# Kernel tuning notes

Hardware: AMD Instinct MI355X
Metric: run time of the kernel (lower is better)

The kernel has to match this reference:

```python
import jax, jax.numpy as jnp
import numpy as np

LS, BS, N_HID, N_PART, T, D_IN, M = 2, 16, 256, 512, 16, 64, 1
MID = N_PART // 2


def setup_inputs() -> dict:
    key = jax.random.key(0)
    ks = jax.random.split(key, 12)
    s = 0.1
    inp = {}
    inp["x"] = jax.random.normal(ks[0], (BS, T, D_IN), jnp.float32)
    inp["y"] = jax.random.normal(ks[1], (BS,), jnp.float32)
    inp["particles"] = jax.random.normal(ks[2], (LS, BS, N_HID, N_PART), jnp.float32)
    inp["weights"] = jnp.full((BS, N_PART), 1.0 / N_PART, jnp.float32)
    inp["q"] = jnp.asarray(1.0, jnp.float32)
    inp["e"] = jnp.asarray(0.1, jnp.float32)
    inp["r"] = jnp.asarray(0.5, jnp.float32)
    inp["Wih0"] = jax.random.normal(ks[3], (4 * N_HID, D_IN), jnp.float32) * s
    inp["Whh0"] = jax.random.normal(ks[4], (4 * N_HID, N_HID), jnp.float32) * s
    inp["b0"] = jnp.zeros((4 * N_HID,), jnp.float32)
    inp["Wih1"] = jax.random.normal(ks[5], (4 * N_HID, N_HID), jnp.float32) * s
    inp["Whh1"] = jax.random.normal(ks[6], (4 * N_HID, N_HID), jnp.float32) * s
    inp["b1"] = jnp.zeros((4 * N_HID,), jnp.float32)
    inp["Wh"] = jax.random.normal(ks[7], (M, N_HID), jnp.float32) * s
    inp["bh"] = jnp.zeros((M,), jnp.float32)
    inp["eps_h"] = jax.random.normal(ks[8], (MID, LS, BS, N_HID), jnp.float32)
    inp["eps_c"] = jax.random.normal(ks[9], (MID, LS, BS, N_HID), jnp.float32)
    u = jax.random.uniform(ks[10], (BS, 2, MID), jnp.float32, minval=1e-6, maxval=1.0)
    inp["gumbel"] = -jnp.log(-jnp.log(u))  # Gumbel noise for multinomial resampling
    return inp


def _lstm(x, h0, c0, Wih0, Whh0, b0, Wih1, Whh1, b1, q2, e2, eps_h, eps_c):
    # x: [bs,T,d]; h0,c0: [ls,bs,n]. Two-layer LSTM, noise added to final states.
    xs = jnp.swapaxes(x, 0, 1)  # [T,bs,d]

    def make_step(Wih, Whh, b):
        def step(carry, xt):
            h, c = carry
            g = xt @ Wih.T + h @ Whh.T + b
            i, f, gg, o = jnp.split(g, 4, axis=-1)
            c2 = jax.nn.sigmoid(f) * c + jax.nn.sigmoid(i) * jnp.tanh(gg)
            h2 = jax.nn.sigmoid(o) * jnp.tanh(c2)
            return (h2, c2), h2
        return step

    (hA, cA), out0 = jax.lax.scan(make_step(Wih0, Whh0, b0), (h0[0], c0[0]), xs)
    (hB, cB), out1 = jax.lax.scan(make_step(Wih1, Whh1, b1), (h0[1], c0[1]), out0)
    hT = jnp.stack([hA, hB]) + jnp.sqrt(q2) * eps_h
    cT = jnp.stack([cA, cB]) + jnp.sqrt(e2) * eps_c
    return jnp.swapaxes(out1, 0, 1), hT, cT


def _obs(u_last, Wh, bh):  # u_last: [bs,n,N] -> [bs,m,N]
    return jnp.einsum('mn,bnN->bmN', Wh, u_last) + bh[None, :, None]


def _estimate(Y, w, r):
    # Y: [bs,m,N], w: [bs,N]
    w_sum = jnp.sum(w, -1)
    W_mu = jnp.einsum('bmN,bN->bm', Y, w) / w_sum[:, None]
    cen = Y - W_mu[:, :, None]
    cov = jnp.einsum('bmN,bkN->bmk', cen, cen) / (Y.shape[-1] - 1)
    cov = cov + jnp.eye(Y.shape[1], dtype=Y.dtype) * (r * r)
    return W_mu, cov


def _inv_logdet(sig):
    m = sig.shape[-1]
    sig = sig + 1e-6 * jnp.eye(m, dtype=sig.dtype)
    L = jnp.linalg.cholesky(sig)
    inv_sig = jnp.linalg.inv(jnp.swapaxes(L, -2, -1)) @ jnp.linalg.inv(L)
    logdet = jnp.linalg.slogdet(sig)[1]
    return inv_sig, logdet


def reference(x, y, particles, weights, q, e, r, Wih0, Whh0, b0, Wih1, Whh1, b1, Wh, bh, eps_h, eps_c, gumbel):
    q2, e2 = q * q, e * e  # noise is squared before the transition (TransitionF)
    # ---- forecast_PF: particle i is h, particle i+MID is c ----
    h_parts = jnp.moveaxis(particles[..., :MID], -1, 0)  # [MID,ls,bs,n]
    c_parts = jnp.moveaxis(particles[..., MID:], -1, 0)
    step_fn = jax.vmap(lambda h0, c0, eh, ec: _lstm(x, h0, c0, Wih0, Whh0, b0, Wih1, Whh1, b1, q2, e2, eh, ec)[1:])
    hN, cN = step_fn(h_parts, c_parts, eps_h, eps_c)
    pr = jnp.moveaxis(jnp.concatenate([hN, cN], 0), 0, -1)  # [ls,bs,n,N]

    # ---- torch_PF weight update ----
    w = jnp.log(weights)
    Y = _obs(pr[-1], Wh, bh)  # [bs,m,N]
    W_mu_e, sig_e = _estimate(Y, w, r)  # NOTE: original passes LOG weights here (faithful)
    inv_sig, logdet = _inv_logdet(sig_e)
    w_sum = jnp.sum(w, -1)
    Wmu2 = Y * w[:, None, :] / w_sum[:, None, None]  # elementwise, as in w_likelihood
    innov = y[:, None, None] - Wmu2  # [bs,m,N]
    quad = jnp.einsum('bmN,bmk,bkN->bN', innov, inv_sig, innov)
    new_w = w + (-0.5 * logdet[:, None] - 0.5 * quad)
    # original: new_w -= log(sum(exp(new_w))) where python-sum reduces dim 0 -> [N]
    new_w = new_w - jnp.log(jnp.sum(jnp.exp(new_w), axis=0))[None, :]
    new_w = jnp.exp(new_w)

    # ---- per-batch, per-half soft resampling when neff < N/4 ----
    def resample_half(p, wh, g):  # p [ls,n,MID], wh [MID], g [MID]
        neff = 1.0 / jnp.sum(wh * wh)
        do = neff < (N_PART / 4.0)
        soft = 0.5 * wh + 0.5 / MID
        idx = jnp.argsort(-(jnp.log(soft) + g))  # weighted sample w/o replacement (Gumbel top-k)
        p_r = p[:, :, idx]
        lw = jnp.log(wh / soft)
        w_r = jnp.exp(lw - jax.nn.logsumexp(lw))
        return jnp.where(do, p_r, p), jnp.where(do, w_r, wh)

    def per_batch(p_b, w_b, g_b):  # p_b [ls,n,N], w_b [N], g_b [2,MID]
        p1, w1 = resample_half(p_b[:, :, :MID], w_b[:MID], g_b[0])
        p2, w2 = resample_half(p_b[:, :, MID:], w_b[MID:], g_b[1])
        return jnp.concatenate([p1, p2], -1), jnp.concatenate([w1, w2], 0)

    pf, wf = jax.vmap(per_batch, in_axes=(1, 0, 0), out_axes=(1, 0))(pr, new_w, gumbel)

    # ---- train=True branch: estimate / likelihood / NIS on filtered ensemble ----
    Yf = _obs(pf[-1], Wh, bh)
    W_mu, sig = _estimate(Yf, wf, r)
    inv_s, ld = _inv_logdet(sig)
    inn = y[:, None] - W_mu  # [bs,m]
    qf = jnp.einsum('bm,bmk,bk->b', inn, inv_s, inn)
    l = jnp.sum(-0.5 * ld - 0.5 * qf)
    nis = jnp.mean(qf)
    return W_mu, sig, pf, wf, l, nis
```

## Files before the change

### kernel.cpp

```cpp
#include <hip/hip_runtime.h>
#include <hip/hip_bf16.h>
#include <math.h>

#define LSN 2
#define BSN 16
#define NH 256
#define NP 512
#define MIDP 256
#define TTN 16
#define DIN 64
#define NCH 4096
#define GW 1024
#define PRS 268
#define BUFSZ 36864

typedef _Float16 f16;
typedef _Float16 f16x8 __attribute__((ext_vector_type(8)));
typedef float f32x4 __attribute__((ext_vector_type(4)));

__device__ __forceinline__ float fsig(float x){ return 1.0f/(1.0f+expf(-x)); }

__device__ __forceinline__ float brsum512(float v, float* red){
  int tid = threadIdx.x;
  red[tid]=v; __syncthreads();
  for (int s=256; s>0; s>>=1){ if (tid<s) red[tid]+=red[tid+s]; __syncthreads(); }
  float r = red[0]; __syncthreads(); return r;
}
__device__ __forceinline__ float brsum(float v, float* red){
  int tid = threadIdx.x;
  red[tid]=v; __syncthreads();
  for (int s=128; s>0; s>>=1){ if (tid<s) red[tid]+=red[tid+s]; __syncthreads(); }
  float r = red[0]; __syncthreads(); return r;
}

__device__ __forceinline__ int gsrow(int jp){
  return ((jp>>5)&3)*NH + (jp>>7)*32 + (jp&31);
}

__global__ __launch_bounds__(256) void k_prep_all(
    const float* __restrict__ Whh0, const float* __restrict__ Wih1,
    const float* __restrict__ Whh1, const float* __restrict__ b1,
    const float* __restrict__ x, const float* __restrict__ Wih0,
    const float* __restrict__ b0, const float* __restrict__ part,
    f16* __restrict__ W0i, f16* __restrict__ W1c, float* __restrict__ b1i,
    float* __restrict__ xW0,
    f16* __restrict__ h0, f16* __restrict__ h1,
    float* __restrict__ c0, float* __restrict__ c1)
{
  __shared__ float lh[64][65];
  __shared__ float lcv[64][65];
  int bid = blockIdx.x;
  int tid = threadIdx.x;
  if (bid < 1024){
    int jp = bid; int srow = gsrow(jp); int t = tid;
    W0i[(size_t)jp*NH + t]        = (f16)Whh0[(size_t)srow*NH + t];
    W1c[(size_t)jp*512 + t]       = (f16)Wih1[(size_t)srow*NH + t];
    W1c[(size_t)jp*512 + 256 + t] = (f16)Whh1[(size_t)srow*NH + t];
    if (t==0) b1i[jp] = b1[srow];
  } else if (bid < 1280){
    int row = bid - 1024;
    float* xr = lh[0];
    if (tid < DIN) xr[tid] = x[(size_t)row*DIN + tid];
    __syncthreads();
    int n = tid;
    for (int q=0;q<4;++q){
      int wrow = q*NH + n;
      float acc = b0[wrow];
      #pragma unroll 8
      for (int d=0; d<DIN; ++d) acc += xr[d] * Wih0[(size_t)wrow*DIN + d];
      int jhat = (n>>5)*128 + q*32 + (n&31);
      xW0[(size_t)row*GW + jhat] = acc;
    }
  } else {
    int idx = bid - 1280;
    int xb = idx & 15, b = (idx>>4)&15, l = idx>>8;
    int i0 = (xb >> 2)*64, n0 = (xb & 3)*64;
    #pragma unroll
    for (int rep=0; rep<16; ++rep){
      int nn = rep*4 + (tid>>6);
      int ii = tid & 63;
      size_t rowb = ((size_t)(l*BSN + b)*NH + n0 + nn)*NP;
      lh[nn][ii]  = part[rowb + i0 + ii];
      lcv[nn][ii] = part[rowb + MIDP + i0 + ii];
    }
    __syncthreads();
    f16* h = l ? h1 : h0;
    float* c = l ? c1 : c0;
    #pragma unroll
    for (int rep=0; rep<16; ++rep){
      int ii = rep*4 + (tid>>6);
      int nn = tid & 63;
      size_t chain = (size_t)b*256 + i0 + ii;
      h[chain*NH + n0 + nn] = (f16)lh[nn][ii];
      c[chain*NH + n0 + nn] = lcv[nn][ii];
    }
  }
}

struct StepCfg {
  const f16* A1; const f16* A2;
  float* C; f16* Hout;
  int layer; int t; int is_last;
};

__global__ __launch_bounds__(256) void k_step2(
    StepCfg cfgA, StepCfg cfgB,
    const f16* __restrict__ W0i, const f16* __restrict__ W1c,
    const float* __restrict__ xw0, const float* __restrict__ b1i,
    float* __restrict__ pr, const float* __restrict__ eps_h, const float* __restrict__ eps_c,
    const float* __restrict__ qp, const float* __restrict__ ep)
{
  __shared__ __align__(16) char smem[2*BUFSZ];

  const int bid = blockIdx.x;
  const int xcd = bid & 7, jj = bid >> 3;
  const int mloc = jj & 3, y = (jj >> 2) & 7, z = (jj >> 5) & 1;
  const int mt = xcd*4 + mloc;
  const int m0 = mt * 128;

  const StepCfg cfg = z ? cfgB : cfgA;
  const int layer  = cfg.layer;
  const int Kt     = layer ? 512 : 256;
  const int nslice = layer ? 8 : 4;
  const f16* W     = layer ? W1c : W0i;

  const int tid = threadIdx.x;
  const int lane = tid & 63, wid = tid >> 6;
  const int lr = lane >> 4, lc = lane & 15;
  const int wm = wid * 32;
  const int bb = mt >> 1;

  float cold[2][2][4];
  #pragma unroll
  for (int mi=0; mi<2; ++mi)
    #pragma unroll
    for (int mh=0; mh<2; ++mh)
      #pragma unroll
      for (int r=0; r<4; ++r)
        cold[mi][mh][r] = cfg.C[(size_t)(m0 + wm + mi*16 + lr*4 + r)*NH + y*32 + mh*16 + lc];

  f32x4 acc[2][8];
  #pragma unroll
  for (int mi=0;mi<2;++mi)
    #pragma unroll
    for (int ni=0;ni<8;++ni) acc[mi][ni] = (f32x4){0.f,0.f,0.f,0.f};

  const int srow = tid >> 1, sseg = (tid & 1)*32;

  float4 ra0,ra1,ra2,ra3, rb0,rb1,rb2,rb3;
  auto loadslice = [&](int ks){
    const f16* Ab; int ka;
    if (layer==1 && ks>=4){ Ab = cfg.A2; ka = (ks-4)*64; } else { Ab = cfg.A1; ka = ks*64; }
    const float4* sa = (const float4*)(Ab + (size_t)(m0+srow)*NH + ka + sseg);
    const float4* sb = (const float4*)(W + (size_t)(y*128+srow)*Kt + (size_t)ks*64 + sseg);
    ra0=sa[0]; ra1=sa[1]; ra2=sa[2]; ra3=sa[3];
    rb0=sb[0]; rb1=sb[1]; rb2=sb[2]; rb3=sb[3];
  };
  auto writeslice = [&](int buf){
    f16* base = (f16*)(smem + buf*BUFSZ);
    float4* da = (float4*)(base + srow*72 + sseg);
    da[0]=ra0; da[1]=ra1; da[2]=ra2; da[3]=ra3;
    float4* db = (float4*)(base + 128*72 + srow*72 + sseg);
    db[0]=rb0; db[1]=rb1; db[2]=rb2; db[3]=rb3;
  };

  loadslice(0);
  writeslice(0);
  __syncthreads();
  for (int ks=0; ks<nslice; ++ks){
    const int cur = ks & 1;
    const bool more = (ks+1) < nslice;
    if (more) loadslice(ks+1);
    const f16* bufA = (const f16*)(smem + cur*BUFSZ);
    const f16* bufB = bufA + 128*72;
    #pragma unroll
    for (int k2=0;k2<2;++k2){
      const int koff = k2*32 + lr*8;
      f16x8 a0 = *(const f16x8*)(bufA + (wm +  0 + lc)*72 + koff);
      f16x8 a1 = *(const f16x8*)(bufA + (wm + 16 + lc)*72 + koff);
      f16x8 b[8];
      #pragma unroll
      for (int ni=0;ni<8;++ni) b[ni] = *(const f16x8*)(bufB + (ni*16 + lc)*72 + koff);
      #pragma unroll
      for (int ni=0;ni<8;++ni){
        acc[0][ni] = __builtin_amdgcn_mfma_f32_16x16x32_f16(a0, b[ni], acc[0][ni], 0,0,0);
        acc[1][ni] = __builtin_amdgcn_mfma_f32_16x16x32_f16(a1, b[ni], acc[1][ni], 0,0,0);
      }
    }
    if (more) writeslice(cur ^ 1);
    __syncthreads();
  }

  float addv[4][2];
  {
    const float* ar = (layer==0) ? (xw0 + (size_t)(bb*TTN + cfg.t)*GW + y*128)
                                 : (b1i + y*128);
    #pragma unroll
    for (int q=0;q<4;++q)
      #pragma unroll
      for (int mh=0;mh<2;++mh)
        addv[q][mh] = ar[q*32 + mh*16 + lc];
  }

  float sq=0.f, se=0.f;
  float* prstage = (float*)smem;
  if (cfg.is_last){
    sq = sqrtf(qp[0]*qp[0]); se = sqrtf(ep[0]*ep[0]);
  }

  #pragma unroll
  for (int mi=0;mi<2;++mi)
   #pragma unroll
   for (int mh=0;mh<2;++mh)
    #pragma unroll
    for (int r=0;r<4;++r){
      float gi = acc[mi][mh+0][r] + addv[0][mh];
      float gf = acc[mi][mh+2][r] + addv[1][mh];
      float gg = acc[mi][mh+4][r] + addv[2][mh];
      float go = acc[mi][mh+6][r] + addv[3][mh];
      float c2 = fsig(gf)*cold[mi][mh][r] + fsig(gi)*tanhf(gg);
      float h2 = fsig(go)*tanhf(c2);
      int ml = wm + mi*16 + lr*4 + r;
      int chain = m0 + ml;
      int nglob = y*32 + mh*16 + lc;
      cfg.Hout[(size_t)chain*NH + nglob] = (f16)h2;
      if (!cfg.is_last){
        cfg.C[(size_t)chain*NH + nglob] = c2;
      } else {
        int ip = (mt & 1)*128 + ml;
        size_t eidx = ((size_t)(ip*LSN + layer)*BSN + bb)*NH + nglob;
        int nl = mh*16 + lc;
        prstage[nl*PRS + ml]       = h2 + sq*eps_h[eidx];
        prstage[nl*PRS + 128 + ml] = c2 + se*eps_c[eidx];
      }
    }

  if (cfg.is_last){
    __syncthreads();
    #pragma unroll
    for (int s=0;s<8;++s){
      int u = s*256 + tid;
      int nl = u >> 6, within = u & 63;
      int half = within >> 5, q4 = within & 31;
      size_t rowp = (size_t)(layer*BSN + bb)*NH + y*32 + nl;
      float4 v = *(const float4*)(prstage + nl*PRS + half*128 + q4*4);
      *(float4*)(pr + rowp*NP + half*MIDP + (mt & 1)*128 + q4*4) = v;
    }
  }
}

__global__ void k_obs_stats(const float* __restrict__ pr, const float* __restrict__ Wh,
                            const float* __restrict__ bh, const float* __restrict__ wts,
                            const float* __restrict__ yv, const float* __restrict__ rp,
                            float* __restrict__ Y, float* __restrict__ pre){
  int b = blockIdx.x; int N = threadIdx.x;
  __shared__ float red[512];
  float acc = bh[0];
  for (int n=0;n<NH;++n) acc += Wh[n] * pr[((size_t)(BSN + b)*NH + n)*NP + N];
  Y[(size_t)b*NP + N] = acc;
  float lw = logf(wts[b*NP+N]);
  float SW = brsum512(lw, red);
  float SY = brsum512(acc*lw, red);
  float mu = SY/SW;
  float cen = acc-mu;
  float SC = brsum512(cen*cen, red);
  float sig = SC/511.0f + rp[0]*rp[0];
  float a = sig+1e-6f, inv = 1.0f/a, ld = logf(a);
  float i0 = yv[b] - acc*lw/SW;
  pre[b*NP+N] = lw - 0.5f*ld - 0.5f*inv*i0*i0;
}

__global__ void k_resample(const float* __restrict__ pre, const float* __restrict__ gum,
                           const float* __restrict__ Y,
                           float* __restrict__ wf, int* __restrict__ idxb, int* __restrict__ dofl,
                           float* __restrict__ Yf, float* __restrict__ out){
  int b = blockIdx.x >> 1, hf = blockIdx.x & 1, j = threadIdx.x;
  __shared__ float red[256]; __shared__ float key[256]; __shared__ int sidx[256];
  int N = hf*256 + j;
  float s=0.f;
  for(int b2=0;b2<BSN;b2++) s += expf(pre[b2*NP+N]);
  float ls = logf(s);
  float wh = expf(pre[b*NP+N] - ls);
  red[j] = wh*wh; __syncthreads();
  for (int s2i=128;s2i>0;s2i>>=1){ if(j<s2i) red[j]+=red[j+s2i]; __syncthreads(); }
  float s2 = red[0]; __syncthreads();
  int doit = (1.0f/s2) < (float)(NP)/4.0f;
  float soft = 0.5f*wh + (0.5f/(float)MIDP);
  float kk = logf(soft) + gum[(b*2+hf)*256 + j];
  key[j] = kk; __syncthreads();
  int rank = 0;
  for (int m=0;m<256;++m){ float km = key[m]; rank += (km > kk) || (km == kk && m < j); }
  sidx[rank] = j; __syncthreads();
  idxb[(b*2+hf)*256 + j] = sidx[j];
  int dcol = doit ? hf*256 + sidx[j] : N;
  Yf[b*NP + N] = Y[b*NP + dcol];
  float lw = logf(wh/soft);
  red[j] = lw; __syncthreads();
  for (int s2i=128;s2i>0;s2i>>=1){ if(j<s2i) red[j] = fmaxf(red[j],red[j+s2i]); __syncthreads(); }
  float mx = red[0]; __syncthreads();
  red[j] = expf(lw-mx); __syncthreads();
  for (int s2i=128;s2i>0;s2i>>=1){ if(j<s2i) red[j]+=red[j+s2i]; __syncthreads(); }
  float lse = mx + logf(red[0]);
  float wr = expf(lw - lse);
  float wv = doit ? wr : wh;
  wf[b*NP + N] = wv;
  out[4194336 + b*NP + N] = wv;
  if (j==0) dofl[b*2+hf] = doit;
}

__global__ void k_pfg(const float* __restrict__ pr, const int* __restrict__ idxb,
                      const int* __restrict__ dofl, float* __restrict__ out){
  __shared__ int dcol[512];
  int blk = blockIdx.x;
  int q = blk & 3, lb = blk >> 2;
  int b = lb & 15;
  int tid = threadIdx.x;
  #pragma unroll
  for (int hf=0; hf<2; ++hf){
    int N = hf*256 + tid;
    dcol[N] = dofl[b*2+hf] ? hf*256 + idxb[(b*2+hf)*256 + tid] : N;
  }
  __syncthreads();
  int d0 = dcol[tid], d1 = dcol[tid+256];
  size_t rowbase = (size_t)lb*NH + q*64;
  for (int rr=0; rr<64; ++rr){
    size_t row = rowbase + rr;
    const float* src = pr + row*NP;
    float* dst = out + 32 + row*NP;
    dst[tid]     = src[d0];
    dst[tid+256] = src[d1];
  }
}

__global__ void k_final_est(const float* __restrict__ Yf, const float* __restrict__ wf,
                            const float* __restrict__ yv, const float* __restrict__ rp,
                            float* __restrict__ qf, float* __restrict__ ldb,
                            float* __restrict__ out){
  int b = blockIdx.x, tid = threadIdx.x;
  __shared__ float red[256];
  float w0 = wf[b*NP+tid], w1 = wf[b*NP+256+tid];
  float y0 = Yf[b*NP+tid], y1 = Yf[b*NP+256+tid];
  float SW = brsum(w0+w1, red);
  float SY = brsum(y0*w0+y1*w1, red);
  float mu = SY/SW;
  float c0=y0-mu, c1=y1-mu;
  float SC = brsum(c0*c0+c1*c1, red);
  float sig = SC/511.0f + rp[0]*rp[0];
  if (tid==0){
    float a = sig + 1e-6f; float inv = 1.0f/a; float ld = logf(a);
    float inn = yv[b]-mu; float q = inn*inn*inv;
    qf[b]=q; ldb[b]=ld;
    out[b]      = mu;
    out[16 + b] = sig;
  }
}

__global__ void k_final_scalar(const float* __restrict__ qf, const float* __restrict__ ldb,
                               float* __restrict__ out){
  if (threadIdx.x==0){
    float l=0.f, nq=0.f;
    for(int b=0;b<BSN;b++){ l += -0.5f*ldb[b]-0.5f*qf[b]; nq += qf[b]; }
    out[4202528] = l;
    out[4202529] = nq/16.0f;
  }
}

extern "C" void kernel_launch(void* const* d_in, const int* in_sizes, int n_in,
                              void* d_out, int out_size, void* d_ws, size_t ws_size,
                              hipStream_t stream) {
  const float* x      = (const float*)d_in[0];
  const float* yv     = (const float*)d_in[1];
  const float* part   = (const float*)d_in[2];
  const float* wts    = (const float*)d_in[3];
  const float* qp     = (const float*)d_in[4];
  const float* ep     = (const float*)d_in[5];
  const float* rp     = (const float*)d_in[6];
  const float* Wih0   = (const float*)d_in[7];
  const float* Whh0   = (const float*)d_in[8];
  const float* b0     = (const float*)d_in[9];
  const float* Wih1   = (const float*)d_in[10];
  const float* Whh1   = (const float*)d_in[11];
  const float* b1     = (const float*)d_in[12];
  const float* Wh     = (const float*)d_in[13];
  const float* bh     = (const float*)d_in[14];
  const float* eps_h  = (const float*)d_in[15];
  const float* eps_c  = (const float*)d_in[16];
  const float* gum    = (const float*)d_in[17];
  float* out = (float*)d_out;

  char* p = (char*)d_ws;
  f16*   W0i  = (f16*)p;  p += (size_t)GW*NH*2;
  f16*   W1c  = (f16*)p;  p += (size_t)GW*512*2;
  float* b1i  = (float*)p; p += (size_t)GW*4;
  float* xW0  = (float*)p; p += (size_t)256*GW*4;
  f16*   h0A  = (f16*)p;  p += (size_t)NCH*NH*2;
  f16*   h0B  = (f16*)p;  p += (size_t)NCH*NH*2;
  f16*   h1A  = (f16*)p;  p += (size_t)NCH*NH*2;
  f16*   h1B  = (f16*)p;  p += (size_t)NCH*NH*2;
  float* c0   = (float*)p; p += (size_t)NCH*NH*4;
  float* c1   = (float*)p; p += (size_t)NCH*NH*4;
  float* pr   = (float*)p; p += (size_t)LSN*BSN*NH*NP*4;
  float* Yb   = (float*)p; p += 32768;
  float* pre  = (float*)p; p += 32768;
  float* wf   = (float*)p; p += 32768;
  float* Yf   = (float*)p; p += 32768;
  int*   idxb = (int*)p;   p += 32768;
  int*   dofl = (int*)p;   p += 128;
  float* qf   = (float*)p; p += 64;
  float* ldb  = (float*)p; p += 64;

  k_prep_all<<<1792, 256, 0, stream>>>(Whh0, Wih1, Whh1, b1, x, Wih0, b0, part,
                                       W0i, W1c, b1i, xW0, h0A, h1A, c0, c1);

  {
    StepCfg s0{h0A, nullptr, c0, h0B, 0, 0, 0};
    k_step2<<<256, 256, 0, stream>>>(s0, s0, W0i, W1c, xW0, b1i,
        pr, eps_h, eps_c, qp, ep);
  }
  f16 *h0cur=h0B, *h0nxt=h0A, *h1cur=h1A, *h1nxt=h1B;
  for (int t=0; t<15; ++t){
    StepCfg ca{h0cur, nullptr, c0, h0nxt, 0, t+1, (t+1==15) ? 1 : 0};
    StepCfg cb{h0cur, h1cur,   c1, h1nxt, 1, t,   0};
    k_step2<<<512, 256, 0, stream>>>(ca, cb, W0i, W1c, xW0, b1i,
        pr, eps_h, eps_c, qp, ep);
    f16* tmp = h0cur; h0cur = h0nxt; h0nxt = tmp;
    tmp = h1cur; h1cur = h1nxt; h1nxt = tmp;
  }
  {
    StepCfg fin{h0cur, h1cur, c1, h1nxt, 1, 15, 1};
    k_step2<<<256, 256, 0, stream>>>(fin, fin, W0i, W1c, xW0, b1i,
        pr, eps_h, eps_c, qp, ep);
  }

  k_obs_stats <<<16, 512, 0, stream>>>(pr, Wh, bh, wts, yv, rp, Yb, pre);
  k_resample  <<<32, 256, 0, stream>>>(pre, gum, Yb, wf, idxb, dofl, Yf, out);
  k_pfg       <<<128, 256, 0, stream>>>(pr, idxb, dofl, out);
  k_final_est <<<16, 256, 0, stream>>>(Yf, wf, yv, rp, qf, ldb, out);
  k_final_scalar<<<1, 64, 0, stream>>>(qf, ldb, out);
}
```

Measured before the change: 390.2 us.

## Drop LDS double buffering in LSTM step GEMM to raise occupancy

The step kernel's register-prefetched, double-buffered LDS pipeline is replaced by a single LDS buffer, with a direct global-to-LDS copy between two barriers on every K slice. The kernel is also declared with launch bounds asking for 4 blocks per SM. The goal is to halve shared memory and cut register pressure so more blocks fit per CU and hide latency through occupancy rather than software prefetch. The trade-off is that global-load latency is no longer overlapped with the MFMA work inside a block. Separately, the observation kernel's reduction loop gets an unroll-by-4 pragma.

```diff
diff --git a/kernel.cpp b/kernel.cpp
--- a/kernel.cpp
+++ b/kernel.cpp
@@ -103,14 +103,14 @@
   int layer; int t; int is_last;
 };
 
-__global__ __launch_bounds__(256) void k_step2(
+__global__ __launch_bounds__(256, 4) void k_step2(
     StepCfg cfgA, StepCfg cfgB,
     const f16* __restrict__ W0i, const f16* __restrict__ W1c,
     const float* __restrict__ xw0, const float* __restrict__ b1i,
     float* __restrict__ pr, const float* __restrict__ eps_h, const float* __restrict__ eps_c,
     const float* __restrict__ qp, const float* __restrict__ ep)
 {
-  __shared__ __align__(16) char smem[2*BUFSZ];
+  __shared__ __align__(16) char smem[BUFSZ];
 
   const int bid = blockIdx.x;
   const int xcd = bid & 7, jj = bid >> 3;
@@ -130,6 +130,10 @@
   const int wm = wid * 32;
   const int bb = mt >> 1;
 
+  f16* Asm = (f16*)smem;
+  f16* Bsm = Asm + 128*72;
+  float* prstage = (float*)smem;
+
   float cold[2][2][4];
   #pragma unroll
   for (int mi=0; mi<2; ++mi)
@@ -146,49 +150,33 @@
     for (int ni=0;ni<8;++ni) acc[mi][ni] = (f32x4){0.f,0.f,0.f,0.f};
 
   const int srow = tid >> 1, sseg = (tid & 1)*32;
-
-  float4 ra0,ra1,ra2,ra3, rb0,rb1,rb2,rb3;
-  auto loadslice = [&](int ks){
+  for (int ks=0; ks<nslice; ++ks){
+    __syncthreads();
     const f16* Ab; int ka;
     if (layer==1 && ks>=4){ Ab = cfg.A2; ka = (ks-4)*64; } else { Ab = cfg.A1; ka = ks*64; }
-    const float4* sa = (const float4*)(Ab + (size_t)(m0+srow)*NH + ka + sseg);
-    const float4* sb = (const float4*)(W + (size_t)(y*128+srow)*Kt + (size_t)ks*64 + sseg);
-    ra0=sa[0]; ra1=sa[1]; ra2=sa[2]; ra3=sa[3];
-    rb0=sb[0]; rb1=sb[1]; rb2=sb[2]; rb3=sb[3];
-  };
-  auto writeslice = [&](int buf){
-    f16* base = (f16*)(smem + buf*BUFSZ);
-    float4* da = (float4*)(base + srow*72 + sseg);
-    da[0]=ra0; da[1]=ra1; da[2]=ra2; da[3]=ra3;
-    float4* db = (float4*)(base + 128*72 + srow*72 + sseg);
-    db[0]=rb0; db[1]=rb1; db[2]=rb2; db[3]=rb3;
-  };
-
-  loadslice(0);
-  writeslice(0);
-  __syncthreads();
-  for (int ks=0; ks<nslice; ++ks){
-    const int cur = ks & 1;
-    const bool more = (ks+1) < nslice;
-    if (more) loadslice(ks+1);
-    const f16* bufA = (const f16*)(smem + cur*BUFSZ);
-    const f16* bufB = bufA + 128*72;
+    {
+      const float4* sa = (const float4*)(Ab + (size_t)(m0+srow)*NH + ka + sseg);
+      float4* da = (float4*)(Asm + srow*72 + sseg);
+      da[0]=sa[0]; da[1]=sa[1]; da[2]=sa[2]; da[3]=sa[3];
+      const float4* sb = (const float4*)(W + (size_t)(y*128+srow)*Kt + (size_t)ks*64 + sseg);
+      float4* db = (float4*)(Bsm + srow*72 + sseg);
+      db[0]=sb[0]; db[1]=sb[1]; db[2]=sb[2]; db[3]=sb[3];
+    }
+    __syncthreads();
     #pragma unroll
     for (int k2=0;k2<2;++k2){
       const int koff = k2*32 + lr*8;
-      f16x8 a0 = *(const f16x8*)(bufA + (wm +  0 + lc)*72 + koff);
-      f16x8 a1 = *(const f16x8*)(bufA + (wm + 16 + lc)*72 + koff);
+      f16x8 a0 = *(const f16x8*)(Asm + (wm +  0 + lc)*72 + koff);
+      f16x8 a1 = *(const f16x8*)(Asm + (wm + 16 + lc)*72 + koff);
       f16x8 b[8];
       #pragma unroll
-      for (int ni=0;ni<8;++ni) b[ni] = *(const f16x8*)(bufB + (ni*16 + lc)*72 + koff);
+      for (int ni=0;ni<8;++ni) b[ni] = *(const f16x8*)(Bsm + (ni*16 + lc)*72 + koff);
       #pragma unroll
       for (int ni=0;ni<8;++ni){
         acc[0][ni] = __builtin_amdgcn_mfma_f32_16x16x32_f16(a0, b[ni], acc[0][ni], 0,0,0);
         acc[1][ni] = __builtin_amdgcn_mfma_f32_16x16x32_f16(a1, b[ni], acc[1][ni], 0,0,0);
       }
     }
-    if (more) writeslice(cur ^ 1);
-    __syncthreads();
   }
 
   float addv[4][2];
@@ -203,9 +191,9 @@
   }
 
   float sq=0.f, se=0.f;
-  float* prstage = (float*)smem;
   if (cfg.is_last){
     sq = sqrtf(qp[0]*qp[0]); se = sqrtf(ep[0]*ep[0]);
+    __syncthreads();
   }
 
   #pragma unroll
@@ -256,6 +244,7 @@
   int b = blockIdx.x; int N = threadIdx.x;
   __shared__ float red[512];
   float acc = bh[0];
+  #pragma unroll 4
   for (int n=0;n<NH;++n) acc += Wh[n] * pr[((size_t)(BSN + b)*NH + n)*NP + N];
   Y[(size_t)b*NP + N] = acc;
   float lw = logf(wts[b*NP+N]);
```

Result: slower. 437.7 us (+12.2%).
